# Kernel optimization log

Hardware: AMD Instinct MI355X
Metric: run time of the kernel (lower is better)

Reference implementation:

```python
import jax, jax.numpy as jnp
import numpy as np

B, NP, NG = 4, 8192, 8192

def setup_inputs() -> dict:
    key = jax.random.key(0)
    k1, k2, k3 = jax.random.split(key, 3)
    pr_pts = jax.random.normal(k1, (B, NP, 3), dtype=jnp.float32)
    gt_pts = jax.random.normal(k2, (B, NG, 3), dtype=jnp.float32)
    gt_valid = jax.random.randint(k3, (B, NG), 0, 2) > 0
    return {"pr_pts": pr_pts, "gt_pts": gt_pts, "gt_valid": gt_valid}

def _sq_dists(a, b):
    # a: [B,N,3], b: [B,M,3] -> squared pairwise distances [B,N,M]
    a2 = jnp.sum(a * a, -1)  # [B,N]
    b2 = jnp.sum(b * b, -1)  # [B,M]
    ab = jnp.einsum('bnd,bmd->bnm', a, b)
    return a2[:, :, None] + b2[:, None, :] - 2.0 * ab

def reference(pr_pts, gt_pts, gt_valid):
    # Bidirectional Chamfer distance with gt validity mask.
    d2 = _sq_dists(pr_pts, gt_pts)  # [B,Np,Ng]
    # accuracy: for each predicted point, min squared dist to a VALID gt point
    d2_masked = jnp.where(gt_valid[:, None, :], d2, jnp.inf)
    acc_b = jnp.mean(jnp.min(d2_masked, axis=-1), axis=-1)  # [B]
    # completeness: for each valid gt point, min squared dist to any pred point
    min_over_pr = jnp.min(d2, axis=1)  # [B,Ng]
    valid_f = gt_valid.astype(min_over_pr.dtype)
    com_b = jnp.sum(min_over_pr * valid_f, axis=-1) / jnp.maximum(jnp.sum(valid_f, axis=-1), 1.0)
    loss_acc = jnp.mean(acc_b)
    loss_com = jnp.mean(com_b)
    loss_cd = loss_acc + loss_com
    # Sum((loss_acc,None),(loss_com,None),(loss_cd,None)) with scalar losses -> acc+com+cd
    return loss_acc + loss_com + loss_cd
```

## Files before the change

### kernel.cpp

```cpp
#include <hip/hip_runtime.h>

#define BB 4
#define NN 8192

typedef _Float16 f16;
typedef _Float16 f16x8 __attribute__((ext_vector_type(8)));
typedef float f32x16 __attribute__((ext_vector_type(16)));

#define SZ_PACK (BB * NN * 16)
#define OFF_PROW_BYTES (2 * SZ_PACK * 2)
#define SZ_PROW (BB * 8 * NN)
#define OFF_PCOL_BYTES (OFF_PROW_BYTES + SZ_PROW * 4)
#define SZ_PCOL (BB * 32 * NN)
#define OFF_RES_BYTES (OFF_PCOL_BYTES + SZ_PCOL * 4)

__global__ __launch_bounds__(256) void k_init(
    const float* __restrict__ pr, const float* __restrict__ gt,
    const int* __restrict__ valid,
    f16* __restrict__ APR, f16* __restrict__ BGT, float* __restrict__ res) {
  int i = blockIdx.x * 256 + threadIdx.x;
  if (blockIdx.x == 0 && threadIdx.x < 16) res[threadIdx.x] = 0.0f;
  if (i >= BB * NN) return;
  float px = pr[3 * i], py = pr[3 * i + 1], pz = pr[3 * i + 2];
  float gx = gt[3 * i], gy = gt[3 * i + 1], gz = gt[3 * i + 2];
  int vld = valid[i] != 0;

  f16 phx = (f16)px, phy = (f16)py, phz = (f16)pz;
  f16 plx = (f16)(px - (float)phx), ply = (f16)(py - (float)phy), plz = (f16)(pz - (float)phz);
  float p2 = px * px + py * py + pz * pz;
  f16 p2h = (f16)p2, p2l = (f16)(p2 - (float)p2h);

  f16 ghx = (f16)gx, ghy = (f16)gy, ghz = (f16)gz;
  f16 glx = (f16)(gx - (float)ghx), gly = (f16)(gy - (float)ghy), glz = (f16)(gz - (float)ghz);
  float g2 = gx * gx + gy * gy + gz * gz;
  f16 g2h = (f16)g2, g2l = (f16)(g2 - (float)g2h);
  f16 g2hm = vld ? g2h : (f16)32768.0f;
  f16 g2lm = vld ? g2l : (f16)0.0f;

  const f16 one = (f16)1.0f, zero = (f16)0.0f;
  union Rec { f16 h[16]; uint4 u[2]; };

  Rec ra;
  ra.h[0] = (f16)(-2.f * (float)phx); ra.h[1] = (f16)(-2.f * (float)phy); ra.h[2] = (f16)(-2.f * (float)phz);
  ra.h[3] = ra.h[0]; ra.h[4] = ra.h[1]; ra.h[5] = ra.h[2];
  ra.h[6] = (f16)(-2.f * (float)plx); ra.h[7] = (f16)(-2.f * (float)ply); ra.h[8] = (f16)(-2.f * (float)plz);
  ra.h[9] = p2h; ra.h[10] = p2l; ra.h[11] = one; ra.h[12] = one;
  ra.h[13] = zero; ra.h[14] = zero; ra.h[15] = zero;
  ((uint4*)APR)[2 * i] = ra.u[0]; ((uint4*)APR)[2 * i + 1] = ra.u[1];

  Rec rd;
  rd.h[0] = ghx; rd.h[1] = ghy; rd.h[2] = ghz;
  rd.h[3] = glx; rd.h[4] = gly; rd.h[5] = glz;
  rd.h[6] = ghx; rd.h[7] = ghy; rd.h[8] = ghz;
  rd.h[9] = one; rd.h[10] = one; rd.h[11] = g2hm; rd.h[12] = g2lm;
  rd.h[13] = zero; rd.h[14] = zero; rd.h[15] = zero;
  ((uint4*)BGT)[2 * i] = rd.u[0]; ((uint4*)BGT)[2 * i + 1] = rd.u[1];
}

__device__ __forceinline__ float min16(const f32x16& d) {
  float v = fminf(fminf(d[0], d[1]), d[2]);
  v = fminf(fminf(v, d[3]), d[4]);
  v = fminf(fminf(v, d[5]), d[6]);
  v = fminf(fminf(v, d[7]), d[8]);
  v = fminf(fminf(v, d[9]), d[10]);
  v = fminf(fminf(v, d[11]), d[12]);
  v = fminf(fminf(v, d[13]), d[14]);
  return fminf(v, d[15]);
}

__global__ __launch_bounds__(256, 4) void k_dist(
    const f16* __restrict__ APR, const f16* __restrict__ BGT,
    float* __restrict__ prow, float* __restrict__ pcol) {
  __shared__ f16 ldsB[2 * 512 * 8];
  __shared__ float colmin_s[4][512];
  int id = blockIdx.x;
  int wgrow  = id & 31;
  int eighth = (id >> 5) & 7;
  int b      = id >> 8;
  int tid = threadIdx.x;
  int wave = tid >> 6, lane = tid & 63;
  int nn = lane & 31, q = lane >> 5;

  const f16* Ab = APR + ((size_t)b * NN + wgrow * 256 + wave * 64 + nn) * 16 + q * 8;
  f16x8 af0 = *(const f16x8*)Ab;
  f16x8 af1 = *(const f16x8*)(Ab + 32 * 16);

  f32x16 zc = {};
  f32x16 m0, m1;
#pragma unroll
  for (int i = 0; i < 16; ++i) { m0[i] = 1e38f; m1[i] = 1e38f; }

  const uint4* gsrc = (const uint4*)(BGT + ((size_t)b * NN + eighth * 1024) * 16);
  uint4* ldsu = (uint4*)ldsB;
  const f16x8* lf = (const f16x8*)ldsB;

  for (int chunk = 0; chunk < 2; ++chunk) {
    const uint4* src = gsrc + chunk * 1024;
#pragma unroll
    for (int k = 0; k < 4; ++k) {
      int u = tid + 256 * k;
      ldsu[(u & 1) * 512 + (u >> 1)] = src[u];
    }
    __syncthreads();
    f16x8 b0 = lf[q * 512 + 0 * 32 + nn];
    f16x8 b1 = lf[q * 512 + 1 * 32 + nn];
    for (int t = 0; t < 16; t += 2) {
      int tn = (t + 2) & 15;
      f16x8 nb0 = lf[q * 512 + tn * 32 + nn];
      f16x8 nb1 = lf[q * 512 + (tn + 1) * 32 + nn];
      f32x16 d0 = __builtin_amdgcn_mfma_f32_32x32x16_f16(af0, b0, zc, 0, 0, 0);
      f32x16 d1 = __builtin_amdgcn_mfma_f32_32x32x16_f16(af0, b1, zc, 0, 0, 0);
#pragma unroll
      for (int i = 0; i < 16; ++i) m0[i] = fminf(fminf(d0[i], d1[i]), m0[i]);
      float c00 = min16(d0), c01 = min16(d1);
      f32x16 d2 = __builtin_amdgcn_mfma_f32_32x32x16_f16(af1, b0, zc, 0, 0, 0);
      f32x16 d3 = __builtin_amdgcn_mfma_f32_32x32x16_f16(af1, b1, zc, 0, 0, 0);
#pragma unroll
      for (int i = 0; i < 16; ++i) m1[i] = fminf(fminf(d2[i], d3[i]), m1[i]);
      float c0 = fminf(c00, min16(d2));
      float c1 = fminf(c01, min16(d3));
      c0 = fminf(c0, __shfl_xor(c0, 32, 64));
      c1 = fminf(c1, __shfl_xor(c1, 32, 64));
      if (q == 0) {
        colmin_s[wave][t * 32 + nn] = c0;
        colmin_s[wave][(t + 1) * 32 + nn] = c1;
      }
      b0 = nb0; b1 = nb1;
    }
    __syncthreads();
    float* pc = pcol + ((size_t)b * 32 + wgrow) * NN + eighth * 1024 + chunk * 512;
#pragma unroll
    for (int e = 0; e < 2; ++e) {
      int c = tid + 256 * e;
      float v = fminf(fminf(colmin_s[0][c], colmin_s[1][c]),
                      fminf(colmin_s[2][c], colmin_s[3][c]));
      pc[c] = fmaxf(v, 0.0f);
    }
  }

#pragma unroll
  for (int i = 0; i < 16; ++i) {
    float v = m0[i];
    v = fminf(v, __shfl_xor(v, 1, 64));
    v = fminf(v, __shfl_xor(v, 2, 64));
    v = fminf(v, __shfl_xor(v, 4, 64));
    v = fminf(v, __shfl_xor(v, 8, 64));
    v = fminf(v, __shfl_xor(v, 16, 64));
    m0[i] = fmaxf(v, 0.0f);
    v = m1[i];
    v = fminf(v, __shfl_xor(v, 1, 64));
    v = fminf(v, __shfl_xor(v, 2, 64));
    v = fminf(v, __shfl_xor(v, 4, 64));
    v = fminf(v, __shfl_xor(v, 8, 64));
    v = fminf(v, __shfl_xor(v, 16, 64));
    m1[i] = fmaxf(v, 0.0f);
  }
  float* pb = prow + ((size_t)b * 8 + eighth) * NN + wgrow * 256 + wave * 64;
#pragma unroll
  for (int reg = 0; reg < 16; ++reg) {
    int rit = (reg & 3) + 8 * (reg >> 2) + 4 * q;
    if (nn == reg) { pb[rit] = m0[reg]; pb[32 + rit] = m1[reg]; }
  }
}

__global__ __launch_bounds__(256) void k_red(
    const float* __restrict__ prow, const float* __restrict__ pcol,
    const int* __restrict__ valid, float* __restrict__ res) {
  int bid = blockIdx.x, tid = threadIdx.x;
  __shared__ float r1[256], r2[256];
  float sum = 0.0f, cnt = 0.0f;
  if (bid < 32) {
    int bb = bid >> 3, seg = bid & 7;
#pragma unroll
    for (int k = 0; k < 4; ++k) {
      int r = seg * 1024 + tid + 256 * k;
      const float* p = prow + (size_t)bb * 8 * NN + r;
      float v = p[0];
#pragma unroll
      for (int e = 1; e < 8; ++e) v = fminf(v, p[(size_t)e * NN]);
      sum += v;
    }
    r1[tid] = sum;
    __syncthreads();
    for (int off = 128; off > 0; off >>= 1) {
      if (tid < off) r1[tid] += r1[tid + off];
      __syncthreads();
    }
    if (tid == 0) atomicAdd(&res[bb], r1[0]);
  } else {
    int g = bid - 32;
    int bb = g >> 4, seg = g & 15;
#pragma unroll
    for (int k = 0; k < 2; ++k) {
      int j = seg * 512 + tid + 256 * k;
      const float* p = pcol + (size_t)bb * 32 * NN + j;
      float v = p[0];
#pragma unroll
      for (int w = 1; w < 32; ++w) v = fminf(v, p[(size_t)w * NN]);
      int vld = valid[bb * NN + j] != 0;
      sum += vld ? v : 0.0f;
      cnt += vld ? 1.0f : 0.0f;
    }
    r1[tid] = sum; r2[tid] = cnt;
    __syncthreads();
    for (int off = 128; off > 0; off >>= 1) {
      if (tid < off) { r1[tid] += r1[tid + off]; r2[tid] += r2[tid + off]; }
      __syncthreads();
    }
    if (tid == 0) {
      atomicAdd(&res[4 + bb], r1[0]);
      atomicAdd(&res[8 + bb], r2[0]);
    }
  }
}

__global__ void k_final(const float* __restrict__ res, float* __restrict__ out) {
  if (threadIdx.x == 0 && blockIdx.x == 0) {
    float a = 0.f, c = 0.f;
    for (int bb = 0; bb < 4; ++bb) {
      a += res[bb] / (float)NN;
      c += res[4 + bb] / fmaxf(res[8 + bb], 1.0f);
    }
    out[0] = 0.5f * (a + c);
  }
}

extern "C" void kernel_launch(void* const* d_in, const int* in_sizes, int n_in,
                              void* d_out, int out_size, void* d_ws, size_t ws_size,
                              hipStream_t stream) {
  const float* pr    = (const float*)d_in[0];
  const float* gt    = (const float*)d_in[1];
  const int*   valid = (const int*)d_in[2];

  f16* base = (f16*)d_ws;
  f16* APR = base;
  f16* BGT = base + SZ_PACK;
  float* prow = (float*)((char*)d_ws + OFF_PROW_BYTES);
  float* pcol = (float*)((char*)d_ws + OFF_PCOL_BYTES);
  float* res  = (float*)((char*)d_ws + OFF_RES_BYTES);

  k_init<<<(BB * NN) / 256, 256, 0, stream>>>(pr, gt, valid, APR, BGT, res);
  k_dist<<<1024, 256, 0, stream>>>(APR, BGT, prow, pcol);
  k_red<<<96, 256, 0, stream>>>(prow, pcol, valid, res);
  k_final<<<1, 64, 0, stream>>>(res, (float*)d_out);
}
```

Before: 87.81 us.

## Fuse fp16 packing into distance kernel and fold final reduction into k_red

Removes the separate packing kernel: each distance block now builds its fp16 hi/lo A fragments straight from the fp32 predicted points and packs the gt records into LDS itself. The final scalar kernel is dropped in favour of a last-block-done atomic counter inside the reduction kernel, and the workspace is zeroed from the distance kernel. This cuts two kernel launches and the packed-buffer round trip through global memory, at the cost of redundant packing work across blocks (each gt tile is repacked by 32 row blocks). The min16 tree is also rebalanced to shorten its dependency chain.

```diff
diff --git a/kernel.cpp b/kernel.cpp
--- a/kernel.cpp
+++ b/kernel.cpp
@@ -7,70 +7,43 @@
 typedef _Float16 f16x8 __attribute__((ext_vector_type(8)));
 typedef float f32x16 __attribute__((ext_vector_type(16)));
 
-#define SZ_PACK (BB * NN * 16)
-#define OFF_PROW_BYTES (2 * SZ_PACK * 2)
 #define SZ_PROW (BB * 8 * NN)
-#define OFF_PCOL_BYTES (OFF_PROW_BYTES + SZ_PROW * 4)
+#define OFF_PCOL_BYTES (SZ_PROW * 4)
 #define SZ_PCOL (BB * 32 * NN)
 #define OFF_RES_BYTES (OFF_PCOL_BYTES + SZ_PCOL * 4)
 
-__global__ __launch_bounds__(256) void k_init(
-    const float* __restrict__ pr, const float* __restrict__ gt,
-    const int* __restrict__ valid,
-    f16* __restrict__ APR, f16* __restrict__ BGT, float* __restrict__ res) {
-  int i = blockIdx.x * 256 + threadIdx.x;
-  if (blockIdx.x == 0 && threadIdx.x < 16) res[threadIdx.x] = 0.0f;
-  if (i >= BB * NN) return;
-  float px = pr[3 * i], py = pr[3 * i + 1], pz = pr[3 * i + 2];
-  float gx = gt[3 * i], gy = gt[3 * i + 1], gz = gt[3 * i + 2];
-  int vld = valid[i] != 0;
-
+union Rec { f16 h[16]; uint4 u[2]; };
+
+__device__ __forceinline__ float min16(const f32x16& d) {
+  float a = fminf(fminf(d[0], d[1]), d[2]);
+  float b = fminf(fminf(d[3], d[4]), d[5]);
+  float c = fminf(fminf(d[6], d[7]), d[8]);
+  float e = fminf(fminf(d[9], d[10]), d[11]);
+  float f = fminf(fminf(d[12], d[13]), d[14]);
+  a = fminf(fminf(a, b), c);
+  e = fminf(fminf(e, f), d[15]);
+  return fminf(a, e);
+}
+
+__device__ __forceinline__ f16x8 make_afrag(const float* __restrict__ pr,
+                                            size_t idx, int q) {
+  float px = pr[3 * idx], py = pr[3 * idx + 1], pz = pr[3 * idx + 2];
   f16 phx = (f16)px, phy = (f16)py, phz = (f16)pz;
   f16 plx = (f16)(px - (float)phx), ply = (f16)(py - (float)phy), plz = (f16)(pz - (float)phz);
   float p2 = px * px + py * py + pz * pz;
   f16 p2h = (f16)p2, p2l = (f16)(p2 - (float)p2h);
-
-  f16 ghx = (f16)gx, ghy = (f16)gy, ghz = (f16)gz;
-  f16 glx = (f16)(gx - (float)ghx), gly = (f16)(gy - (float)ghy), glz = (f16)(gz - (float)ghz);
-  float g2 = gx * gx + gy * gy + gz * gz;
-  f16 g2h = (f16)g2, g2l = (f16)(g2 - (float)g2h);
-  f16 g2hm = vld ? g2h : (f16)32768.0f;
-  f16 g2lm = vld ? g2l : (f16)0.0f;
-
-  const f16 one = (f16)1.0f, zero = (f16)0.0f;
-  union Rec { f16 h[16]; uint4 u[2]; };
-
-  Rec ra;
-  ra.h[0] = (f16)(-2.f * (float)phx); ra.h[1] = (f16)(-2.f * (float)phy); ra.h[2] = (f16)(-2.f * (float)phz);
-  ra.h[3] = ra.h[0]; ra.h[4] = ra.h[1]; ra.h[5] = ra.h[2];
-  ra.h[6] = (f16)(-2.f * (float)plx); ra.h[7] = (f16)(-2.f * (float)ply); ra.h[8] = (f16)(-2.f * (float)plz);
-  ra.h[9] = p2h; ra.h[10] = p2l; ra.h[11] = one; ra.h[12] = one;
-  ra.h[13] = zero; ra.h[14] = zero; ra.h[15] = zero;
-  ((uint4*)APR)[2 * i] = ra.u[0]; ((uint4*)APR)[2 * i + 1] = ra.u[1];
-
-  Rec rd;
-  rd.h[0] = ghx; rd.h[1] = ghy; rd.h[2] = ghz;
-  rd.h[3] = glx; rd.h[4] = gly; rd.h[5] = glz;
-  rd.h[6] = ghx; rd.h[7] = ghy; rd.h[8] = ghz;
-  rd.h[9] = one; rd.h[10] = one; rd.h[11] = g2hm; rd.h[12] = g2lm;
-  rd.h[13] = zero; rd.h[14] = zero; rd.h[15] = zero;
-  ((uint4*)BGT)[2 * i] = rd.u[0]; ((uint4*)BGT)[2 * i + 1] = rd.u[1];
-}
-
-__device__ __forceinline__ float min16(const f32x16& d) {
-  float v = fminf(fminf(d[0], d[1]), d[2]);
-  v = fminf(fminf(v, d[3]), d[4]);
-  v = fminf(fminf(v, d[5]), d[6]);
-  v = fminf(fminf(v, d[7]), d[8]);
-  v = fminf(fminf(v, d[9]), d[10]);
-  v = fminf(fminf(v, d[11]), d[12]);
-  v = fminf(fminf(v, d[13]), d[14]);
-  return fminf(v, d[15]);
+  f16 ax = (f16)(-2.f * (float)phx), ay = (f16)(-2.f * (float)phy), az = (f16)(-2.f * (float)phz);
+  f16 lx = (f16)(-2.f * (float)plx), ly = (f16)(-2.f * (float)ply), lz = (f16)(-2.f * (float)plz);
+  f16x8 lo = {ax, ay, az, ax, ay, az, lx, ly};
+  f16x8 hi = {lz, p2h, p2l, (f16)1.f, (f16)1.f, (f16)0.f, (f16)0.f, (f16)0.f};
+  return q ? hi : lo;
 }
 
 __global__ __launch_bounds__(256, 4) void k_dist(
-    const f16* __restrict__ APR, const f16* __restrict__ BGT,
-    float* __restrict__ prow, float* __restrict__ pcol) {
+    const float* __restrict__ pr, const float* __restrict__ gt,
+    const int* __restrict__ valid,
+    float* __restrict__ prow, float* __restrict__ pcol,
+    float* __restrict__ res) {
   __shared__ f16 ldsB[2 * 512 * 8];
   __shared__ float colmin_s[4][512];
   int id = blockIdx.x;
@@ -81,25 +54,41 @@
   int wave = tid >> 6, lane = tid & 63;
   int nn = lane & 31, q = lane >> 5;
 
-  const f16* Ab = APR + ((size_t)b * NN + wgrow * 256 + wave * 64 + nn) * 16 + q * 8;
-  f16x8 af0 = *(const f16x8*)Ab;
-  f16x8 af1 = *(const f16x8*)(Ab + 32 * 16);
+  if (id == 0 && tid < 17) res[tid] = 0.0f;
+
+  size_t arow = (size_t)b * NN + wgrow * 256 + wave * 64 + nn;
+  f16x8 af0 = make_afrag(pr, arow, q);
+  f16x8 af1 = make_afrag(pr, arow + 32, q);
 
   f32x16 zc = {};
   f32x16 m0, m1;
 #pragma unroll
   for (int i = 0; i < 16; ++i) { m0[i] = 1e38f; m1[i] = 1e38f; }
 
-  const uint4* gsrc = (const uint4*)(BGT + ((size_t)b * NN + eighth * 1024) * 16);
   uint4* ldsu = (uint4*)ldsB;
   const f16x8* lf = (const f16x8*)ldsB;
 
   for (int chunk = 0; chunk < 2; ++chunk) {
-    const uint4* src = gsrc + chunk * 1024;
-#pragma unroll
-    for (int k = 0; k < 4; ++k) {
-      int u = tid + 256 * k;
-      ldsu[(u & 1) * 512 + (u >> 1)] = src[u];
+    int colbase = eighth * 1024 + chunk * 512;
+#pragma unroll
+    for (int rr = 0; rr < 2; ++rr) {
+      int j = tid + 256 * rr;
+      size_t gi = (size_t)b * NN + colbase + j;
+      float gx = gt[3 * gi], gy = gt[3 * gi + 1], gz = gt[3 * gi + 2];
+      int vld = valid[gi] != 0;
+      f16 ghx = (f16)gx, ghy = (f16)gy, ghz = (f16)gz;
+      f16 glx = (f16)(gx - (float)ghx), gly = (f16)(gy - (float)ghy), glz = (f16)(gz - (float)ghz);
+      float g2 = gx * gx + gy * gy + gz * gz;
+      f16 g2h = (f16)g2, g2l = (f16)(g2 - (float)g2h);
+      Rec rd;
+      rd.h[0] = ghx; rd.h[1] = ghy; rd.h[2] = ghz;
+      rd.h[3] = glx; rd.h[4] = gly; rd.h[5] = glz;
+      rd.h[6] = ghx; rd.h[7] = ghy; rd.h[8] = ghz;
+      rd.h[9] = (f16)1.f; rd.h[10] = (f16)1.f;
+      rd.h[11] = vld ? g2h : (f16)32768.0f;
+      rd.h[12] = vld ? g2l : (f16)0.0f;
+      rd.h[13] = (f16)0.f; rd.h[14] = (f16)0.f; rd.h[15] = (f16)0.f;
+      ldsu[j] = rd.u[0]; ldsu[512 + j] = rd.u[1];
     }
     __syncthreads();
     f16x8 b0 = lf[q * 512 + 0 * 32 + nn];
@@ -165,7 +154,8 @@
 
 __global__ __launch_bounds__(256) void k_red(
     const float* __restrict__ prow, const float* __restrict__ pcol,
-    const int* __restrict__ valid, float* __restrict__ res) {
+    const int* __restrict__ valid, float* __restrict__ res,
+    float* __restrict__ out) {
   int bid = blockIdx.x, tid = threadIdx.x;
   __shared__ float r1[256], r2[256];
   float sum = 0.0f, cnt = 0.0f;
@@ -212,16 +202,19 @@
       atomicAdd(&res[8 + bb], r2[0]);
     }
   }
-}
-
-__global__ void k_final(const float* __restrict__ res, float* __restrict__ out) {
-  if (threadIdx.x == 0 && blockIdx.x == 0) {
-    float a = 0.f, c = 0.f;
-    for (int bb = 0; bb < 4; ++bb) {
-      a += res[bb] / (float)NN;
-      c += res[4 + bb] / fmaxf(res[8 + bb], 1.0f);
-    }
-    out[0] = 0.5f * (a + c);
+  if (tid == 0) {
+    __threadfence();
+    unsigned t = atomicAdd((unsigned*)&res[16], 1u);
+    if (t == 95u) {
+      float a = 0.f, c = 0.f;
+      for (int bb2 = 0; bb2 < 4; ++bb2) {
+        a += atomicAdd(&res[bb2], 0.0f) * (1.0f / (float)NN);
+        float s = atomicAdd(&res[4 + bb2], 0.0f);
+        float n = atomicAdd(&res[8 + bb2], 0.0f);
+        c += s / fmaxf(n, 1.0f);
+      }
+      out[0] = 0.5f * (a + c);
+    }
   }
 }
 
@@ -232,15 +225,10 @@
   const float* gt    = (const float*)d_in[1];
   const int*   valid = (const int*)d_in[2];
 
-  f16* base = (f16*)d_ws;
-  f16* APR = base;
-  f16* BGT = base + SZ_PACK;
-  float* prow = (float*)((char*)d_ws + OFF_PROW_BYTES);
+  float* prow = (float*)d_ws;
   float* pcol = (float*)((char*)d_ws + OFF_PCOL_BYTES);
   float* res  = (float*)((char*)d_ws + OFF_RES_BYTES);
 
-  k_init<<<(BB * NN) / 256, 256, 0, stream>>>(pr, gt, valid, APR, BGT, res);
-  k_dist<<<1024, 256, 0, stream>>>(APR, BGT, prow, pcol);
-  k_red<<<96, 256, 0, stream>>>(prow, pcol, valid, res);
-  k_final<<<1, 64, 0, stream>>>(res, (float*)d_out);
-}
+  k_dist<<<1024, 256, 0, stream>>>(pr, gt, valid, prow, pcol, res);
+  k_red<<<96, 256, 0, stream>>>(prow, pcol, valid, res, (float*)d_out);
+}
```

Result: slower. 91.12 us (+3.8%).
